# Kernel tuning notes

Measured on AMD Instinct MI355X. Metric: run time of the kernel, lower is better.

The kernel has to match this reference:

```python
import jax, jax.numpy as jnp
import numpy as np

B, N, F_IN, F_OUT = 8, 2048, 256, 256
H, D = 8, 32
LN_EPS = 1e-5


def setup_inputs() -> dict:
    key = jax.random.key(0)
    ks = jax.random.split(key, 8)
    s = 1.0 / np.sqrt(F_IN)
    so = 1.0 / np.sqrt(H * D)
    return {
        "x": jax.random.normal(ks[0], (B, N, F_IN), dtype=jnp.float32),
        "adj": jax.random.randint(ks[1], (B, N, N), 0, 2, dtype=jnp.int32),
        "Wq": jax.random.uniform(ks[2], (F_IN, H * D), jnp.float32, -s, s),
        "bq": jnp.zeros((H * D,), jnp.float32),
        "Wk": jax.random.uniform(ks[3], (F_IN, H * D), jnp.float32, -s, s),
        "bk": jnp.zeros((H * D,), jnp.float32),
        "Wv": jax.random.uniform(ks[4], (F_IN, H * D), jnp.float32, -s, s),
        "bv": jnp.zeros((H * D,), jnp.float32),
        "Wo": jax.random.uniform(ks[5], (H * D, F_OUT), jnp.float32, -so, so),
        "bo": jnp.zeros((F_OUT,), jnp.float32),
        "gamma": jnp.ones((F_OUT,), jnp.float32),
        "beta": jnp.zeros((F_OUT,), jnp.float32),
    }


def reference(x, adj, Wq, bq, Wk, bk, Wv, bv, Wo, bo, gamma, beta):
    b, n, _ = x.shape
    # QKV projections -> [B, H, N, D]
    q = (x @ Wq + bq).reshape(b, n, H, D).transpose(0, 2, 1, 3)
    k = (x @ Wk + bk).reshape(b, n, H, D).transpose(0, 2, 1, 3)
    v = (x @ Wv + bv).reshape(b, n, H, D).transpose(0, 2, 1, 3)
    # masked attention scores [B, H, N, N]
    scores = jnp.einsum('bhqd,bhkd->bhqk', q, k) / np.sqrt(D).astype(np.float32)
    scores = jnp.where(adj[:, None, :, :] == 0, -jnp.inf, scores)
    attn = jax.nn.softmax(scores, axis=-1)
    # dropout layers are identity in eval mode
    out = jnp.einsum('bhqk,bhkd->bhqd', attn, v)
    out = out.transpose(0, 2, 1, 3).reshape(b, n, H * D)
    out = out @ Wo + bo
    # LayerNorm
    mu = out.mean(-1, keepdims=True)
    var = out.var(-1, keepdims=True)
    out = (out - mu) * jax.lax.rsqrt(var + LN_EPS) * gamma + beta
    return out, attn.mean(axis=1)
```

## Files before the change

### kernel.cpp

```cpp
#include <hip/hip_runtime.h>


typedef __attribute__((ext_vector_type(8))) short short8;
typedef __attribute__((ext_vector_type(4))) float f32x4;
typedef __attribute__((ext_vector_type(4))) unsigned short us4;
typedef unsigned short u16;
typedef unsigned int u32;

#define SC2 0.25503486127240555f
#define MS2 28.853900817779268f

__device__ __forceinline__ float b2f(u16 u) {
  union { u32 i; float f; } v; v.i = ((u32)u) << 16; return v.f;
}
__device__ __forceinline__ u16 cvt(float f) {
  __bf16 h = (__bf16)f;
  union { __bf16 h; u16 u; } v; v.h = h; return v.u;
}

__global__ __launch_bounds__(256) void k_prep(
    const int* __restrict__ adj, u32* __restrict__ packed,
    const float* __restrict__ w0, const float* __restrict__ w1,
    const float* __restrict__ w2, const float* __restrict__ w3,
    u16* __restrict__ o0, u16* __restrict__ o1,
    u16* __restrict__ o2, u16* __restrict__ o3) {
  int bid = blockIdx.x;
  if (bid < 256) {
    int z = bid >> 6, rem = bid & 63;
    const float* in; u16* out;
    if (z == 0) { in = w0; out = o0; }
    else if (z == 1) { in = w1; out = o1; }
    else if (z == 2) { in = w2; out = o2; }
    else { in = w3; out = o3; }
    __shared__ u16 t[32][33];
    int tx = threadIdx.x & 31, ty = threadIdx.x >> 5;
    int x0 = (rem & 7) * 32, y0 = (rem >> 3) * 32;
    for (int j = 0; j < 32; j += 8)
      t[ty + j][tx] = cvt(in[(y0 + ty + j) * 256 + x0 + tx]);
    __syncthreads();
    for (int j = 0; j < 32; j += 8)
      out[(x0 + ty + j) * 256 + y0 + tx] = t[tx][ty + j];
  } else {
    int lane = threadIdx.x & 63;
#pragma unroll 4
    for (int it = 0; it < 64; it++) {
      unsigned int i = ((bid - 256) * 64u + it) * 256u + threadIdx.x;
      unsigned long long m = __ballot(adj[i] != 0);
      if (lane == 0)       packed[i >> 5] = (u32)m;
      else if (lane == 32) packed[i >> 5] = (u32)(m >> 32);
    }
  }
}

__global__ __launch_bounds__(256) void k_qkv(
    const float* __restrict__ x, const u16* __restrict__ wt,
    const float* __restrict__ bq, const float* __restrict__ bk,
    const float* __restrict__ bv,
    u16* __restrict__ qw, u16* __restrict__ kw, u16* __restrict__ vt) {
  int l = threadIdx.x & 63, w = threadIdx.x >> 6;
  int lr = l & 15, lg = l >> 4;
  int row0 = blockIdx.y * 64 + w * 16;
  int c0 = blockIdx.x * 64;
  f32x4 acc[4] = {};
  const float* xr = x + (size_t)(row0 + lr) * 256 + lg * 8;
  const u16* wr = wt + (c0 + lr) * 256 + lg * 8;
  for (int k0 = 0; k0 < 256; k0 += 32) {
    f32x4 f0 = *(const f32x4*)(xr + k0);
    f32x4 f1 = *(const f32x4*)(xr + k0 + 4);
    short8 a;
    a[0] = (short)cvt(f0[0]); a[1] = (short)cvt(f0[1]);
    a[2] = (short)cvt(f0[2]); a[3] = (short)cvt(f0[3]);
    a[4] = (short)cvt(f1[0]); a[5] = (short)cvt(f1[1]);
    a[6] = (short)cvt(f1[2]); a[7] = (short)cvt(f1[3]);
#pragma unroll
    for (int ct = 0; ct < 4; ct++) {
      short8 bb = *(const short8*)(wr + ct * 16 * 256 + k0);
      acc[ct] = __builtin_amdgcn_mfma_f32_16x16x32_bf16(a, bb, acc[ct], 0, 0, 0);
    }
  }
  int mtx = blockIdx.x >> 2;
  const float* bias = (mtx == 0) ? bq : ((mtx == 1) ? bk : bv);
  int b = row0 >> 11, nbase = row0 & 2047;
#pragma unroll
  for (int ct = 0; ct < 4; ct++) {
    int cc = (c0 + ct * 16 + lr) & 255;
    int h = cc >> 5, d = cc & 31;
    float bs = bias[cc];
    if (mtx < 2) {
      u16* dst = (mtx == 0) ? qw : kw;
#pragma unroll
      for (int rr = 0; rr < 4; rr++) {
        int n = nbase + lg * 4 + rr;
        dst[((b * 8 + h) * 2048 + n) * 32 + d] = cvt(acc[ct][rr] + bs);
      }
    } else {
      us4 pk;
#pragma unroll
      for (int rr = 0; rr < 4; rr++) pk[rr] = cvt(acc[ct][rr] + bs);
      *(us4*)(vt + (size_t)((b * 8 + h) * 32 + d) * 2048 + nbase + lg * 4) = pk;
    }
  }
}

__global__ __launch_bounds__(512, 6) void k_attn(
    const u16* __restrict__ qw, const u16* __restrict__ kw,
    const u16* __restrict__ vt, const u32* __restrict__ packed,
    u16* __restrict__ ao, float* __restrict__ out2) {
  __shared__ __align__(16) u16 P[8][2048];
  int l = threadIdx.x & 63, h = threadIdx.x >> 6;
  int lr = l & 15, lg = l >> 4;
  int b = blockIdx.y, q0 = blockIdx.x * 32;
  const u16* qb = qw + (size_t)((b * 8 + h) * 2048 + q0) * 32;
  const u16* kb = kw + (size_t)((b * 8 + h) * 2048) * 32;
  const u16* vb = vt + (size_t)((b * 8 + h) * 32) * 2048;
  short8 qf0 = *(const short8*)(qb + lr * 32 + lg * 8);
  short8 qf1 = *(const short8*)(qb + (16 + lr) * 32 + lg * 8);
  const u32* pkb = packed + (size_t)(b * 2048 + q0) * 64;

  float ls0 = 0.f, ls1 = 0.f;
#pragma unroll 2
  for (int ch = 0; ch < 32; ch++) {
    uint2 m0 = *(const uint2*)(pkb + lr * 64 + ch * 2);
    uint2 m1 = *(const uint2*)(pkb + (16 + lr) * 64 + ch * 2);
#pragma unroll
    for (int j = 0; j < 4; j++) {
      short8 kf = *(const short8*)(kb + (size_t)(ch * 64 + j * 16 + lr) * 32 + lg * 8);
      f32x4 z = {};
      f32x4 s0 = __builtin_amdgcn_mfma_f32_16x16x32_bf16(kf, qf0, z, 0, 0, 0);
      f32x4 s1 = __builtin_amdgcn_mfma_f32_16x16x32_bf16(kf, qf1, z, 0, 0, 0);
      u32 w0 = ((j & 2) ? m0.y : m0.x) >> ((j & 1) * 16 + lg * 4);
      u32 w1 = ((j & 2) ? m1.y : m1.x) >> ((j & 1) * 16 + lg * 4);
#pragma unroll
      for (int rr = 0; rr < 4; rr++) {
        float e0 = __builtin_exp2f(fmaf(s0[rr], SC2, -MS2));
        float e1 = __builtin_exp2f(fmaf(s1[rr], SC2, -MS2));
        ls0 += ((w0 >> rr) & 1u) ? e0 : 0.0f;
        ls1 += ((w1 >> rr) & 1u) ? e1 : 0.0f;
      }
    }
  }
  ls0 += __shfl_xor(ls0, 16); ls0 += __shfl_xor(ls0, 32);
  ls1 += __shfl_xor(ls1, 16); ls1 += __shfl_xor(ls1, 32);
  float lil0 = -__log2f(fmaxf(ls0, 1e-30f)) - MS2;
  float lil1 = -__log2f(fmaxf(ls1, 1e-30f)) - MS2;

  f32x4 acc[2][2] = {};
  for (int ch = 0; ch < 32; ch++) {
    u16* Pt = &P[h][0];
    uint2 m0 = *(const uint2*)(pkb + lr * 64 + ch * 2);
    uint2 m1 = *(const uint2*)(pkb + (16 + lr) * 64 + ch * 2);
#pragma unroll
    for (int j = 0; j < 4; j++) {
      short8 kf = *(const short8*)(kb + (size_t)(ch * 64 + j * 16 + lr) * 32 + lg * 8);
      f32x4 z = {};
      f32x4 s0 = __builtin_amdgcn_mfma_f32_16x16x32_bf16(kf, qf0, z, 0, 0, 0);
      f32x4 s1 = __builtin_amdgcn_mfma_f32_16x16x32_bf16(kf, qf1, z, 0, 0, 0);
      u32 w0 = ((j & 2) ? m0.y : m0.x) >> ((j & 1) * 16 + lg * 4);
      u32 w1 = ((j & 2) ? m1.y : m1.x) >> ((j & 1) * 16 + lg * 4);
      us4 p0, p1;
#pragma unroll
      for (int rr = 0; rr < 4; rr++) {
        float e0 = __builtin_exp2f(fmaf(s0[rr], SC2, lil0));
        float e1 = __builtin_exp2f(fmaf(s1[rr], SC2, lil1));
        p0[rr] = cvt(((w0 >> rr) & 1u) ? e0 : 0.0f);
        p1[rr] = cvt(((w1 >> rr) & 1u) ? e1 : 0.0f);
      }
      int slot = 2 * j + (lg >> 1), offs = (lg & 1) * 4;
      *(us4*)(Pt + lr * 64 + ((slot ^ (lr & 7)) << 3) + offs) = p0;
      *(us4*)(Pt + (16 + lr) * 64 + ((slot ^ (lr & 7)) << 3) + offs) = p1;
    }
#pragma unroll
    for (int k2 = 0; k2 < 2; k2++) {
      short8 pa0 = *(const short8*)(Pt + lr * 64 +
                      (((k2 * 4 + lg) ^ (lr & 7)) << 3));
      short8 pa1 = *(const short8*)(Pt + (16 + lr) * 64 +
                      (((k2 * 4 + lg) ^ (lr & 7)) << 3));
#pragma unroll
      for (int dt = 0; dt < 2; dt++) {
        short8 vf = *(const short8*)(vb + (size_t)(dt * 16 + lr) * 2048 +
                                     ch * 64 + k2 * 32 + lg * 8);
        acc[0][dt] = __builtin_amdgcn_mfma_f32_16x16x32_bf16(pa0, vf, acc[0][dt], 0, 0, 0);
        acc[1][dt] = __builtin_amdgcn_mfma_f32_16x16x32_bf16(pa1, vf, acc[1][dt], 0, 0, 0);
      }
    }
    __syncthreads();
    {
      int t = threadIdx.x;
      int r = t >> 4, c4 = t & 15;
      int addr = r * 64 + (((c4 >> 1) ^ (r & 7)) << 3) + (c4 & 1) * 4;
      float s0 = 0.f, s1 = 0.f, s2 = 0.f, s3 = 0.f;
#pragma unroll
      for (int w8 = 0; w8 < 8; w8++) {
        us4 v = *(const us4*)&P[w8][addr];
        s0 += b2f(v[0]); s1 += b2f(v[1]); s2 += b2f(v[2]); s3 += b2f(v[3]);
      }
      f32x4 o;
      o[0] = s0 * 0.125f; o[1] = s1 * 0.125f;
      o[2] = s2 * 0.125f; o[3] = s3 * 0.125f;
      *(f32x4*)(out2 + (size_t)(b * 2048 + q0 + r) * 2048 + ch * 64 + c4 * 4) = o;
    }
    __syncthreads();
  }
#pragma unroll
  for (int qs = 0; qs < 2; qs++)
#pragma unroll
    for (int dt = 0; dt < 2; dt++)
#pragma unroll
      for (int rr = 0; rr < 4; rr++) {
        int n = q0 + qs * 16 + lg * 4 + rr;
        ao[(size_t)(b * 2048 + n) * 256 + h * 32 + dt * 16 + lr] =
            cvt(acc[qs][dt][rr]);
      }
}

__global__ __launch_bounds__(256) void k_oproj(
    const u16* __restrict__ ao, const u16* __restrict__ wto,
    const float* __restrict__ bo, const float* __restrict__ gamma,
    const float* __restrict__ beta, float* __restrict__ out) {
  int l = threadIdx.x & 63, w = threadIdx.x >> 6;
  int lr = l & 15, lg = l >> 4;
  int row0 = blockIdx.x * 64 + w * 16;
  f32x4 acc[16] = {};
  const u16* ar = ao + (size_t)(row0 + lr) * 256 + lg * 8;
  const u16* wr = wto + lr * 256 + lg * 8;
  for (int k0 = 0; k0 < 256; k0 += 32) {
    short8 a = *(const short8*)(ar + k0);
#pragma unroll
    for (int ct = 0; ct < 16; ct++) {
      short8 bb = *(const short8*)(wr + ct * 16 * 256 + k0);
      acc[ct] = __builtin_amdgcn_mfma_f32_16x16x32_bf16(a, bb, acc[ct], 0, 0, 0);
    }
  }
  float sum[4] = {0, 0, 0, 0}, sq[4] = {0, 0, 0, 0};
#pragma unroll
  for (int ct = 0; ct < 16; ct++) {
    float bs = bo[ct * 16 + lr];
#pragma unroll
    for (int rr = 0; rr < 4; rr++) {
      float v = acc[ct][rr] + bs;
      acc[ct][rr] = v;
      sum[rr] += v; sq[rr] += v * v;
    }
  }
#pragma unroll
  for (int rr = 0; rr < 4; rr++) {
    float s = sum[rr], q = sq[rr];
    s += __shfl_xor(s, 1); s += __shfl_xor(s, 2);
    s += __shfl_xor(s, 4); s += __shfl_xor(s, 8);
    q += __shfl_xor(q, 1); q += __shfl_xor(q, 2);
    q += __shfl_xor(q, 4); q += __shfl_xor(q, 8);
    float mu = s * (1.0f / 256.0f);
    float var = fmaxf(q * (1.0f / 256.0f) - mu * mu, 0.0f);
    sum[rr] = mu;
    sq[rr] = rsqrtf(var + 1e-5f);
  }
#pragma unroll
  for (int ct = 0; ct < 16; ct++) {
    float g = gamma[ct * 16 + lr], be = beta[ct * 16 + lr];
#pragma unroll
    for (int rr = 0; rr < 4; rr++) {
      int n = row0 + lg * 4 + rr;
      out[(size_t)n * 256 + ct * 16 + lr] =
          ((acc[ct][rr] - sum[rr]) * sq[rr]) * g + be;
    }
  }
}

extern "C" void kernel_launch(void* const* d_in, const int* in_sizes, int n_in,
                              void* d_out, int out_size, void* d_ws, size_t ws_size,
                              hipStream_t stream) {
  const float* x    = (const float*)d_in[0];
  const int*   adj  = (const int*)d_in[1];
  const float* Wq   = (const float*)d_in[2];
  const float* bq   = (const float*)d_in[3];
  const float* Wk   = (const float*)d_in[4];
  const float* bk   = (const float*)d_in[5];
  const float* Wv   = (const float*)d_in[6];
  const float* bv   = (const float*)d_in[7];
  const float* Wo   = (const float*)d_in[8];
  const float* bo   = (const float*)d_in[9];
  const float* gamma= (const float*)d_in[10];
  const float* beta = (const float*)d_in[11];

  char* ws = (char*)d_ws;
  u16* wtq = (u16*)(ws + 0);
  u16* wtk = (u16*)(ws + 131072);
  u16* wtv = (u16*)(ws + 262144);
  u16* wto = (u16*)(ws + 393216);
  u16* qw  = (u16*)(ws + 524288);
  u16* kw  = (u16*)(ws + 8912896);
  u16* vt  = (u16*)(ws + 17301504);
  u16* ao  = (u16*)(ws + 25690112);
  u32* pk  = (u32*)(ws + 34078720);

  float* out  = (float*)d_out;
  float* out2 = out + (size_t)8 * 2048 * 256;

  k_prep<<<dim3(2304), dim3(256), 0, stream>>>(adj, pk, Wq, Wk, Wv, Wo,
                                               wtq, wtk, wtv, wto);
  k_qkv<<<dim3(12, 256), dim3(256), 0, stream>>>(x, wtq, bq, bk, bv, qw, kw, vt);
  k_attn<<<dim3(64, 8), dim3(512), 0, stream>>>(qw, kw, vt, pk, ao, out2);
  k_oproj<<<dim3(256), dim3(256), 0, stream>>>(ao, wto, bo, gamma, beta, out);
}
```

Measured before the change: 404.6 us.

## Fuse softmax sum with PV pass and compute head-mean in separate phase

The separate row-sum pass is merged into the PV pass. Unnormalized exp values feed both the running sum and the P·V MFMAs, and the output is divided by the sum at the end. The head-averaged attention map moves to a second phase after a single barrier. In that phase each wave recomputes QK for all heads on its slice and writes fp32 means, which removes the two block-wide syncs per chunk. Q is pre-scaled by the log2 softmax factor in the projection, and the fixed exponent offset is dropped, so large scores could overflow exp2.

```diff
diff --git a/kernel.cpp b/kernel.cpp
--- a/kernel.cpp
+++ b/kernel.cpp
@@ -8,11 +8,7 @@
 typedef unsigned int u32;
 
 #define SC2 0.25503486127240555f
-#define MS2 28.853900817779268f
-
-__device__ __forceinline__ float b2f(u16 u) {
-  union { u32 i; float f; } v; v.i = ((u32)u) << 16; return v.f;
-}
+
 __device__ __forceinline__ u16 cvt(float f) {
   __bf16 h = (__bf16)f;
   union { __bf16 h; u16 u; } v; v.h = h; return v.u;
@@ -88,10 +84,11 @@
     float bs = bias[cc];
     if (mtx < 2) {
       u16* dst = (mtx == 0) ? qw : kw;
+      float sc = (mtx == 0) ? SC2 : 1.0f;
 #pragma unroll
       for (int rr = 0; rr < 4; rr++) {
         int n = nbase + lg * 4 + rr;
-        dst[((b * 8 + h) * 2048 + n) * 32 + d] = cvt(acc[ct][rr] + bs);
+        dst[((b * 8 + h) * 2048 + n) * 32 + d] = cvt((acc[ct][rr] + bs) * sc);
       }
     } else {
       us4 pk;
@@ -102,115 +99,125 @@
   }
 }
 
-__global__ __launch_bounds__(512, 6) void k_attn(
+__global__ __launch_bounds__(512) void k_attn(
     const u16* __restrict__ qw, const u16* __restrict__ kw,
     const u16* __restrict__ vt, const u32* __restrict__ packed,
     u16* __restrict__ ao, float* __restrict__ out2) {
   __shared__ __align__(16) u16 P[8][2048];
-  int l = threadIdx.x & 63, h = threadIdx.x >> 6;
+  __shared__ float lsbuf[8][32];
+  int l = threadIdx.x & 63, wv = threadIdx.x >> 6;
   int lr = l & 15, lg = l >> 4;
   int b = blockIdx.y, q0 = blockIdx.x * 32;
-  const u16* qb = qw + (size_t)((b * 8 + h) * 2048 + q0) * 32;
-  const u16* kb = kw + (size_t)((b * 8 + h) * 2048) * 32;
-  const u16* vb = vt + (size_t)((b * 8 + h) * 32) * 2048;
-  short8 qf0 = *(const short8*)(qb + lr * 32 + lg * 8);
-  short8 qf1 = *(const short8*)(qb + (16 + lr) * 32 + lg * 8);
   const u32* pkb = packed + (size_t)(b * 2048 + q0) * 64;
 
-  float ls0 = 0.f, ls1 = 0.f;
-#pragma unroll 2
-  for (int ch = 0; ch < 32; ch++) {
-    uint2 m0 = *(const uint2*)(pkb + lr * 64 + ch * 2);
-    uint2 m1 = *(const uint2*)(pkb + (16 + lr) * 64 + ch * 2);
-#pragma unroll
-    for (int j = 0; j < 4; j++) {
-      short8 kf = *(const short8*)(kb + (size_t)(ch * 64 + j * 16 + lr) * 32 + lg * 8);
-      f32x4 z = {};
-      f32x4 s0 = __builtin_amdgcn_mfma_f32_16x16x32_bf16(kf, qf0, z, 0, 0, 0);
-      f32x4 s1 = __builtin_amdgcn_mfma_f32_16x16x32_bf16(kf, qf1, z, 0, 0, 0);
-      u32 w0 = ((j & 2) ? m0.y : m0.x) >> ((j & 1) * 16 + lg * 4);
-      u32 w1 = ((j & 2) ? m1.y : m1.x) >> ((j & 1) * 16 + lg * 4);
+  {
+    int h = wv;
+    const u16* qb = qw + (size_t)((b * 8 + h) * 2048 + q0) * 32;
+    const u16* kb = kw + (size_t)((b * 8 + h) * 2048) * 32;
+    const u16* vb = vt + (size_t)((b * 8 + h) * 32) * 2048;
+    short8 qf0 = *(const short8*)(qb + lr * 32 + lg * 8);
+    short8 qf1 = *(const short8*)(qb + (16 + lr) * 32 + lg * 8);
+    u16* Pt = &P[h][0];
+    float ls0 = 0.f, ls1 = 0.f;
+    f32x4 acc[2][2] = {};
+    for (int ch = 0; ch < 32; ch++) {
+      uint2 m0 = *(const uint2*)(pkb + lr * 64 + ch * 2);
+      uint2 m1 = *(const uint2*)(pkb + (16 + lr) * 64 + ch * 2);
+#pragma unroll
+      for (int j = 0; j < 4; j++) {
+        short8 kf = *(const short8*)(kb + (size_t)(ch * 64 + j * 16 + lr) * 32 + lg * 8);
+        f32x4 z = {};
+        f32x4 s0 = __builtin_amdgcn_mfma_f32_16x16x32_bf16(kf, qf0, z, 0, 0, 0);
+        f32x4 s1 = __builtin_amdgcn_mfma_f32_16x16x32_bf16(kf, qf1, z, 0, 0, 0);
+        u32 w0 = ((j & 2) ? m0.y : m0.x) >> ((j & 1) * 16 + lg * 4);
+        u32 w1 = ((j & 2) ? m1.y : m1.x) >> ((j & 1) * 16 + lg * 4);
+        us4 p0, p1;
+#pragma unroll
+        for (int rr = 0; rr < 4; rr++) {
+          float e0 = __builtin_exp2f(s0[rr]);
+          float e1 = __builtin_exp2f(s1[rr]);
+          float em0 = ((w0 >> rr) & 1u) ? e0 : 0.0f;
+          float em1 = ((w1 >> rr) & 1u) ? e1 : 0.0f;
+          ls0 += em0; ls1 += em1;
+          p0[rr] = cvt(em0); p1[rr] = cvt(em1);
+        }
+        int slot = 2 * j + (lg >> 1), offs = (lg & 1) * 4;
+        *(us4*)(Pt + lr * 64 + ((slot ^ (lr & 7)) << 3) + offs) = p0;
+        *(us4*)(Pt + (16 + lr) * 64 + ((slot ^ (lr & 7)) << 3) + offs) = p1;
+      }
+#pragma unroll
+      for (int k2 = 0; k2 < 2; k2++) {
+        short8 pa0 = *(const short8*)(Pt + lr * 64 +
+                        (((k2 * 4 + lg) ^ (lr & 7)) << 3));
+        short8 pa1 = *(const short8*)(Pt + (16 + lr) * 64 +
+                        (((k2 * 4 + lg) ^ (lr & 7)) << 3));
+#pragma unroll
+        for (int dt = 0; dt < 2; dt++) {
+          short8 vf = *(const short8*)(vb + (size_t)(dt * 16 + lr) * 2048 +
+                                       ch * 64 + k2 * 32 + lg * 8);
+          acc[0][dt] = __builtin_amdgcn_mfma_f32_16x16x32_bf16(pa0, vf, acc[0][dt], 0, 0, 0);
+          acc[1][dt] = __builtin_amdgcn_mfma_f32_16x16x32_bf16(pa1, vf, acc[1][dt], 0, 0, 0);
+        }
+      }
+    }
+    ls0 += __shfl_xor(ls0, 16); ls0 += __shfl_xor(ls0, 32);
+    ls1 += __shfl_xor(ls1, 16); ls1 += __shfl_xor(ls1, 32);
+    ls0 = fmaxf(ls0, 1e-30f); ls1 = fmaxf(ls1, 1e-30f);
+    if (l < 16) { lsbuf[h][lr] = ls0; lsbuf[h][16 + lr] = ls1; }
+    float r0 = 1.0f / ls0, r1 = 1.0f / ls1;
+#pragma unroll
+    for (int qs = 0; qs < 2; qs++)
 #pragma unroll
       for (int rr = 0; rr < 4; rr++) {
-        float e0 = __builtin_exp2f(fmaf(s0[rr], SC2, -MS2));
-        float e1 = __builtin_exp2f(fmaf(s1[rr], SC2, -MS2));
-        ls0 += ((w0 >> rr) & 1u) ? e0 : 0.0f;
-        ls1 += ((w1 >> rr) & 1u) ? e1 : 0.0f;
-      }
-    }
-  }
-  ls0 += __shfl_xor(ls0, 16); ls0 += __shfl_xor(ls0, 32);
-  ls1 += __shfl_xor(ls1, 16); ls1 += __shfl_xor(ls1, 32);
-  float lil0 = -__log2f(fmaxf(ls0, 1e-30f)) - MS2;
-  float lil1 = -__log2f(fmaxf(ls1, 1e-30f)) - MS2;
-
-  f32x4 acc[2][2] = {};
-  for (int ch = 0; ch < 32; ch++) {
-    u16* Pt = &P[h][0];
-    uint2 m0 = *(const uint2*)(pkb + lr * 64 + ch * 2);
-    uint2 m1 = *(const uint2*)(pkb + (16 + lr) * 64 + ch * 2);
-#pragma unroll
-    for (int j = 0; j < 4; j++) {
-      short8 kf = *(const short8*)(kb + (size_t)(ch * 64 + j * 16 + lr) * 32 + lg * 8);
-      f32x4 z = {};
-      f32x4 s0 = __builtin_amdgcn_mfma_f32_16x16x32_bf16(kf, qf0, z, 0, 0, 0);
-      f32x4 s1 = __builtin_amdgcn_mfma_f32_16x16x32_bf16(kf, qf1, z, 0, 0, 0);
-      u32 w0 = ((j & 2) ? m0.y : m0.x) >> ((j & 1) * 16 + lg * 4);
-      u32 w1 = ((j & 2) ? m1.y : m1.x) >> ((j & 1) * 16 + lg * 4);
-      us4 p0, p1;
-#pragma unroll
-      for (int rr = 0; rr < 4; rr++) {
-        float e0 = __builtin_exp2f(fmaf(s0[rr], SC2, lil0));
-        float e1 = __builtin_exp2f(fmaf(s1[rr], SC2, lil1));
-        p0[rr] = cvt(((w0 >> rr) & 1u) ? e0 : 0.0f);
-        p1[rr] = cvt(((w1 >> rr) & 1u) ? e1 : 0.0f);
-      }
-      int slot = 2 * j + (lg >> 1), offs = (lg & 1) * 4;
-      *(us4*)(Pt + lr * 64 + ((slot ^ (lr & 7)) << 3) + offs) = p0;
-      *(us4*)(Pt + (16 + lr) * 64 + ((slot ^ (lr & 7)) << 3) + offs) = p1;
-    }
-#pragma unroll
-    for (int k2 = 0; k2 < 2; k2++) {
-      short8 pa0 = *(const short8*)(Pt + lr * 64 +
-                      (((k2 * 4 + lg) ^ (lr & 7)) << 3));
-      short8 pa1 = *(const short8*)(Pt + (16 + lr) * 64 +
-                      (((k2 * 4 + lg) ^ (lr & 7)) << 3));
-#pragma unroll
-      for (int dt = 0; dt < 2; dt++) {
-        short8 vf = *(const short8*)(vb + (size_t)(dt * 16 + lr) * 2048 +
-                                     ch * 64 + k2 * 32 + lg * 8);
-        acc[0][dt] = __builtin_amdgcn_mfma_f32_16x16x32_bf16(pa0, vf, acc[0][dt], 0, 0, 0);
-        acc[1][dt] = __builtin_amdgcn_mfma_f32_16x16x32_bf16(pa1, vf, acc[1][dt], 0, 0, 0);
-      }
-    }
-    __syncthreads();
-    {
-      int t = threadIdx.x;
-      int r = t >> 4, c4 = t & 15;
-      int addr = r * 64 + (((c4 >> 1) ^ (r & 7)) << 3) + (c4 & 1) * 4;
-      float s0 = 0.f, s1 = 0.f, s2 = 0.f, s3 = 0.f;
-#pragma unroll
-      for (int w8 = 0; w8 < 8; w8++) {
-        us4 v = *(const us4*)&P[w8][addr];
-        s0 += b2f(v[0]); s1 += b2f(v[1]); s2 += b2f(v[2]); s3 += b2f(v[3]);
-      }
-      f32x4 o;
-      o[0] = s0 * 0.125f; o[1] = s1 * 0.125f;
-      o[2] = s2 * 0.125f; o[3] = s3 * 0.125f;
-      *(f32x4*)(out2 + (size_t)(b * 2048 + q0 + r) * 2048 + ch * 64 + c4 * 4) = o;
-    }
-    __syncthreads();
-  }
-#pragma unroll
-  for (int qs = 0; qs < 2; qs++)
-#pragma unroll
-    for (int dt = 0; dt < 2; dt++)
-#pragma unroll
-      for (int rr = 0; rr < 4; rr++) {
-        int n = q0 + qs * 16 + lg * 4 + rr;
-        ao[(size_t)(b * 2048 + n) * 256 + h * 32 + dt * 16 + lr] =
-            cvt(acc[qs][dt][rr]);
-      }
+        float rq = __shfl(qs == 0 ? r0 : r1, lg * 4 + rr);
+#pragma unroll
+        for (int dt = 0; dt < 2; dt++) {
+          int n = q0 + qs * 16 + lg * 4 + rr;
+          ao[(size_t)(b * 2048 + n) * 256 + h * 32 + dt * 16 + lr] =
+              cvt(acc[qs][dt][rr] * rq);
+        }
+      }
+  }
+  __syncthreads();
+
+  {
+    int qh = (wv >> 2) * 16;
+    int c0 = (wv & 3) * 8;
+    short8 qfh[8];
+    float lil[8];
+#pragma unroll
+    for (int hh = 0; hh < 8; hh++) {
+      qfh[hh] = *(const short8*)(qw +
+          (size_t)((b * 8 + hh) * 2048 + q0 + qh + lr) * 32 + lg * 8);
+      lil[hh] = -__log2f(lsbuf[hh][qh + lr]);
+    }
+    const u32* pkb2 = packed + (size_t)(b * 2048 + q0 + qh) * 64;
+    for (int ch = c0; ch < c0 + 8; ch++) {
+      uint2 mw = *(const uint2*)(pkb2 + lr * 64 + ch * 2);
+#pragma unroll
+      for (int j = 0; j < 4; j++) {
+        f32x4 macc = {};
+#pragma unroll
+        for (int hh = 0; hh < 8; hh++) {
+          const u16* kbh = kw + (size_t)((b * 8 + hh) * 2048) * 32;
+          short8 kf = *(const short8*)(kbh +
+              (size_t)(ch * 64 + j * 16 + lr) * 32 + lg * 8);
+          f32x4 z = {};
+          f32x4 s = __builtin_amdgcn_mfma_f32_16x16x32_bf16(kf, qfh[hh], z, 0, 0, 0);
+#pragma unroll
+          for (int rr = 0; rr < 4; rr++)
+            macc[rr] += __builtin_exp2f(s[rr] + lil[hh]);
+        }
+        u32 wj = ((j & 2) ? mw.y : mw.x) >> ((j & 1) * 16 + lg * 4);
+        f32x4 o;
+#pragma unroll
+        for (int rr = 0; rr < 4; rr++)
+          o[rr] = ((wj >> rr) & 1u) ? macc[rr] * 0.125f : 0.0f;
+        *(f32x4*)(out2 + (size_t)(b * 2048 + q0 + qh + lr) * 2048 +
+                  ch * 64 + j * 16 + lg * 4) = o;
+      }
+    }
+  }
 }
 
 __global__ __launch_bounds__(256) void k_oproj(
```

Result: faster. 377.0 us (-6.8%).
